# Optimization experiments

Measured on AMD Instinct MI355X. Metric: run time of the kernel, lower is better.

Reference implementation:

```python
import jax, jax.numpy as jnp
import numpy as np

N, M, P = 8192, 8192, 16


def setup_inputs() -> dict:
    key = jax.random.key(0)
    k1, k2, k3, k4, k5 = jax.random.split(key, 5)
    x1 = jax.random.normal(k1, (N, P), dtype=jnp.float32)
    x2 = jax.random.normal(k2, (M, P), dtype=jnp.float32)
    # flax initializers.uniform() draws in [0, 0.01); use small scalars
    log_sigma_b = jax.random.uniform(k3, (), dtype=jnp.float32) * 0.01
    log_sigma_v = jax.random.uniform(k4, (), dtype=jnp.float32) * 0.01
    offset = jax.random.uniform(k5, (), dtype=jnp.float32) * 0.01
    return {"x1": x1, "x2": x2, "log_sigma_b": log_sigma_b,
            "log_sigma_v": log_sigma_v, "offset": offset}


def reference(x1, x2, log_sigma_b, log_sigma_v, offset):
    sigma_b = jnp.exp(log_sigma_b)
    sigma_v = jnp.exp(log_sigma_v)
    # sum_p (x1-offset)(x2-offset) as a dot product (n,p)@(p,m) -> (n,m)
    d = jnp.einsum("np,mp->nm", x1 - offset, x2 - offset)
    K = sigma_v ** 2 * d + sigma_b ** 2
    return K
```

## Files before the change

kernel.cpp:

```cpp
#include <hip/hip_runtime.h>
#include <cmath>


typedef float f32x4 __attribute__((ext_vector_type(4)));

#define ROWS_PER_BLOCK 32
#define BLOCK_COLS 1024

__global__ __launch_bounds__(256, 4) void linear_kernel(
    const float* __restrict__ x1, const float* __restrict__ x2,
    const float* __restrict__ p_lsb, const float* __restrict__ p_lsv,
    const float* __restrict__ p_off, float* __restrict__ out,
    int n, int m)
{
    const int lane = threadIdx.x & 63;
    const int wid  = threadIdx.x >> 6;
    const int c0   = blockIdx.x * BLOCK_COLS + wid * 256 + (lane << 2);
    const int n0   = blockIdx.y * ROWS_PER_BLOCK;

    const float off = p_off[0];
    const float sv  = expf(p_lsv[0]);
    const float sb  = expf(p_lsb[0]);
    const float sv2 = sv * sv;
    const float sb2 = sb * sb;

    float C[4][16];
    f32x4 bias;
    #pragma unroll
    for (int c = 0; c < 4; ++c) {
        const f32x4* g = (const f32x4*)(x2 + (size_t)(c0 + c) * 16);
        float s = 0.0f;
        #pragma unroll
        for (int q = 0; q < 4; ++q) {
            f32x4 v = g[q];
            #pragma unroll
            for (int j = 0; j < 4; ++j) {
                const float t = sv2 * (v[j] - off);
                C[c][q * 4 + j] = t;
                s += t;
            }
        }
        bias[c] = sb2 - off * s;
    }

    float* orow = out + (size_t)n0 * m + c0;
    const f32x4* arow = (const f32x4*)(x1 + (size_t)n0 * 16);

#define FMA4(Av, base)                                                  \
    _Pragma("unroll")                                                   \
    for (int j = 0; j < 4; ++j) {                                       \
        acc[0] = fmaf(Av[j], C[0][(base) + j], acc[0]);                 \
        acc[1] = fmaf(Av[j], C[1][(base) + j], acc[1]);                 \
        acc[2] = fmaf(Av[j], C[2][(base) + j], acc[2]);                 \
        acc[3] = fmaf(Av[j], C[3][(base) + j], acc[3]);                 \
    }

#define COMPUTE_STORE(A0, A1, A2, A3) do {                              \
        f32x4 acc = bias;                                               \
        FMA4(A0, 0) FMA4(A1, 4) FMA4(A2, 8) FMA4(A3, 12)               \
        __builtin_nontemporal_store(acc, (f32x4*)orow);                 \
        orow += m;                                                      \
    } while (0)

    f32x4 a0 = arow[0], a1 = arow[1], a2 = arow[2], a3 = arow[3];
    #pragma unroll
    for (int r = 0; r < ROWS_PER_BLOCK - 1; ++r) {
        const f32x4 b0 = arow[(r + 1) * 4 + 0];
        const f32x4 b1 = arow[(r + 1) * 4 + 1];
        const f32x4 b2 = arow[(r + 1) * 4 + 2];
        const f32x4 b3 = arow[(r + 1) * 4 + 3];
        COMPUTE_STORE(a0, a1, a2, a3);
        a0 = b0; a1 = b1; a2 = b2; a3 = b3;
    }
    COMPUTE_STORE(a0, a1, a2, a3);

#undef COMPUTE_STORE
#undef FMA4
}

extern "C" void kernel_launch(void* const* d_in, const int* in_sizes, int n_in,
                              void* d_out, int out_size, void* d_ws, size_t ws_size,
                              hipStream_t stream) {
    const float* x1  = (const float*)d_in[0];
    const float* x2  = (const float*)d_in[1];
    const float* lsb = (const float*)d_in[2];
    const float* lsv = (const float*)d_in[3];
    const float* off = (const float*)d_in[4];
    float* out = (float*)d_out;

    const int n = in_sizes[0] / 16;
    const int m = in_sizes[1] / 16;

    dim3 grid(m / BLOCK_COLS, n / ROWS_PER_BLOCK);
    linear_kernel<<<grid, 256, 0, stream>>>(x1, x2, lsb, lsv, off, out, n, m);
}
```

Before: 305.6 us.

## Switch to persistent grid-stride kernel over row bands with regular stores

Replaces the 2D grid of 2048 blocks, each doing 32 rows, with a persistent grid of 512 blocks. Each block keeps one column chunk of x2 in registers and strides over 8-row bands of x1, so per-block setup is paid once and launch/tail overhead shrinks. It also swaps the nontemporal stores for ordinary stores and lowers the launch_bounds occupancy hint from 4 to 2. The kernel is dominated by writing a 256 MB output, so the gain hinges on store behaviour, and fewer resident waves may hurt latency hiding.

```diff
diff --git a/kernel.cpp b/kernel.cpp
--- a/kernel.cpp
+++ b/kernel.cpp
@@ -4,10 +4,12 @@
 
 typedef float f32x4 __attribute__((ext_vector_type(4)));
 
-#define ROWS_PER_BLOCK 32
-#define BLOCK_COLS 1024
+#define BLOCK_THREADS 256
+#define CHUNK_COLS    1024
+#define BAND_ROWS     8
+#define GRID_BLOCKS   512
 
-__global__ __launch_bounds__(256, 4) void linear_kernel(
+__global__ __launch_bounds__(256, 2) void linear_kernel(
     const float* __restrict__ x1, const float* __restrict__ x2,
     const float* __restrict__ p_lsb, const float* __restrict__ p_lsv,
     const float* __restrict__ p_off, float* __restrict__ out,
@@ -15,8 +17,14 @@
 {
     const int lane = threadIdx.x & 63;
     const int wid  = threadIdx.x >> 6;
-    const int c0   = blockIdx.x * BLOCK_COLS + wid * 256 + (lane << 2);
-    const int n0   = blockIdx.y * ROWS_PER_BLOCK;
+
+    const int nchunks = m / CHUNK_COLS;
+    const int chunk   = blockIdx.x % nchunks;
+    const int b0      = blockIdx.x / nchunks;
+    const int bstep   = gridDim.x / nchunks;
+    const int nbands  = n / BAND_ROWS;
+
+    const int c0 = chunk * CHUNK_COLS + wid * 256 + (lane << 2);
 
     const float off = p_off[0];
     const float sv  = expf(p_lsv[0]);
@@ -43,9 +51,6 @@
         bias[c] = sb2 - off * s;
     }
 
-    float* orow = out + (size_t)n0 * m + c0;
-    const f32x4* arow = (const f32x4*)(x1 + (size_t)n0 * 16);
-
 #define FMA4(Av, base)                                                  \
     _Pragma("unroll")                                                   \
     for (int j = 0; j < 4; ++j) {                                       \
@@ -55,26 +60,31 @@
         acc[3] = fmaf(Av[j], C[3][(base) + j], acc[3]);                 \
     }
 
-#define COMPUTE_STORE(A0, A1, A2, A3) do {                              \
-        f32x4 acc = bias;                                               \
-        FMA4(A0, 0) FMA4(A1, 4) FMA4(A2, 8) FMA4(A3, 12)               \
-        __builtin_nontemporal_store(acc, (f32x4*)orow);                 \
-        orow += m;                                                      \
-    } while (0)
+    {
+        const f32x4* ar = (const f32x4*)(x1 + (size_t)b0 * BAND_ROWS * 16);
+        f32x4 a0 = ar[0], a1 = ar[1], a2 = ar[2], a3 = ar[3];
 
-    f32x4 a0 = arow[0], a1 = arow[1], a2 = arow[2], a3 = arow[3];
-    #pragma unroll
-    for (int r = 0; r < ROWS_PER_BLOCK - 1; ++r) {
-        const f32x4 b0 = arow[(r + 1) * 4 + 0];
-        const f32x4 b1 = arow[(r + 1) * 4 + 1];
-        const f32x4 b2 = arow[(r + 1) * 4 + 2];
-        const f32x4 b3 = arow[(r + 1) * 4 + 3];
-        COMPUTE_STORE(a0, a1, a2, a3);
-        a0 = b0; a1 = b1; a2 = b2; a3 = b3;
+        for (int b = b0; b < nbands; b += bstep) {
+            const f32x4* arB = (const f32x4*)(x1 + (size_t)b * BAND_ROWS * 16);
+            const int bn = b + bstep;
+            const f32x4* an = (const f32x4*)(
+                x1 + (size_t)(bn < nbands ? bn : b) * BAND_ROWS * 16);
+            float* orow = out + (size_t)b * BAND_ROWS * m + c0;
+
+            #pragma unroll
+            for (int r = 0; r < BAND_ROWS; ++r) {
+                const f32x4* pn = (r < BAND_ROWS - 1) ? (arB + (r + 1) * 4) : an;
+                const f32x4 n0 = pn[0], n1 = pn[1], n2 = pn[2], n3 = pn[3];
+
+                f32x4 acc = bias;
+                FMA4(a0, 0) FMA4(a1, 4) FMA4(a2, 8) FMA4(a3, 12)
+                *(f32x4*)orow = acc;
+                orow += m;
+
+                a0 = n0; a1 = n1; a2 = n2; a3 = n3;
+            }
+        }
     }
-    COMPUTE_STORE(a0, a1, a2, a3);
-
-#undef COMPUTE_STORE
 #undef FMA4
 }
 
@@ -91,6 +101,6 @@
     const int n = in_sizes[0] / 16;
     const int m = in_sizes[1] / 16;
 
-    dim3 grid(m / BLOCK_COLS, n / ROWS_PER_BLOCK);
-    linear_kernel<<<grid, 256, 0, stream>>>(x1, x2, lsb, lsv, off, out, n, m);
+    linear_kernel<<<dim3(GRID_BLOCKS), BLOCK_THREADS, 0, stream>>>(
+        x1, x2, lsb, lsv, off, out, n, m);
 }
```

Result: slower. 319.5 us (+4.6%).
